# Performance work log

Hardware: AMD Instinct MI355X
Metric: run time of the kernel (lower is better)

## Reference

```python
import jax, jax.numpy as jnp
import numpy as np

H = 224  # config.output_height
W = 224  # config.output_width
N = 381  # config.num_frequency_bins (one splat per bin)
B = 16   # frames rendered per batch


def setup_inputs() -> dict:
    key = jax.random.key(0)
    k1, k2, k3 = jax.random.split(key, 3)
    # positions in [-0.9, 0.9] (spiral stays inside the frame)
    positions = jax.random.uniform(k1, (B, N, 2), dtype=jnp.float32, minval=-0.9, maxval=0.9)
    colors = jax.random.uniform(k2, (B, N, 3), dtype=jnp.float32)  # RGB in [0,1]
    # sizes in pixels, matching base_size=2 + size_scale=8*softplus(...)
    sizes = jax.random.uniform(k3, (B, N), dtype=jnp.float32, minval=2.0, maxval=10.0)
    return {"positions": positions, "colors": colors, "sizes": sizes}


def reference(positions, colors, sizes):
    """Soft (differentiable) rasterization of Gaussian point splats.

    positions: [B,N,2] in [-1,1]; colors: [B,N,3] in [0,1]; sizes: [B,N] pixels.
    Returns image [B,H,W,3] in [0,1].
    """
    gy = jnp.linspace(-1.0, 1.0, H, dtype=positions.dtype)
    gx = jnp.linspace(-1.0, 1.0, W, dtype=positions.dtype)
    # squared distance from every pixel to every point: [B,N,H,W]
    dx = gx[None, None, None, :] - positions[:, :, 0, None, None]
    dy = gy[None, None, :, None] - positions[:, :, 1, None, None]
    d2 = dx * dx + dy * dy
    # pixel size -> normalized coords ([-1,1] spans H pixels)
    sigma = sizes * (2.0 / H)  # [B,N]
    inv_two_var = 1.0 / (2.0 * sigma * sigma + 1e-8)
    weights = jnp.exp(-d2 * inv_two_var[:, :, None, None])  # [B,N,H,W]
    image = jnp.einsum('bnhw,bnc->bhwc', weights, colors)   # accumulate splats
    return jnp.clip(image, 0.0, 1.0)
```

## Files before the change

### kernel.cpp

```cpp
#include <hip/hip_runtime.h>
#include <math.h>

#define HH 224
#define WW 224
#define NS 381
#define BB 16
#define NPIX (BB * HH * WW)
#define TPB 256
#define TILE_W 32
#define TILE_H 32
#define TILES_X (WW / TILE_W)
#define BLKS_PER_IMG (TILES_X * (HH / TILE_H))
#define NBLK (BB * BLKS_PER_IMG)
#define NS_PAD 384
#define CUT 19.93f

__global__ __launch_bounds__(256) void splat_prep(const float* __restrict__ pos,
                                                  const float* __restrict__ col,
                                                  const float* __restrict__ siz,
                                                  float4* __restrict__ ws) {
    int i = blockIdx.x * 256 + threadIdx.x;
    if (i >= BB * NS) return;
    float px = pos[2 * i + 0];
    float py = pos[2 * i + 1];
    float cr = col[3 * i + 0];
    float cg = col[3 * i + 1];
    float cb = col[3 * i + 2];
    float sg = siz[i] * (2.0f / (float)HH);
    float itv = 1.0f / (2.0f * sg * sg + 1e-8f);
    float ss = sqrtf(itv * 1.44269504088896340736f);
    ws[2 * i + 0] = make_float4(ss, -px * ss, -py * ss, cr);
    ws[2 * i + 1] = make_float4(cg, cb, 0.0f, 0.0f);
}

__global__ __launch_bounds__(TPB) void splat_render(const float4* __restrict__ ws,
                                                    float* __restrict__ out) {
    __shared__ float4 geo[NS_PAD];
    __shared__ float4 colr[NS_PAD];
    __shared__ int cnt;

    int blk = blockIdx.x;
    int b = blk / BLKS_PER_IMG;
    int t = blk - b * BLKS_PER_IMG;
    int tile_y = t / TILES_X;
    int tile_x = t - tile_y * TILES_X;

    if (threadIdx.x == 0) cnt = 0;
    __syncthreads();

    const float gstep = 2.0f / (float)(WW - 1);
    float x0 = -1.0f + (float)(tile_x * TILE_W) * gstep;
    float x1 = x0 + (float)(TILE_W - 1) * gstep;
    float y0 = -1.0f + (float)(tile_y * TILE_H) * gstep;
    float y1 = y0 + (float)(TILE_H - 1) * gstep;

    const float4* src = ws + (size_t)b * NS * 2;
    int lane = threadIdx.x & 63;

    for (int r = 0; r < 2; ++r) {
        int i = threadIdx.x + r * TPB;
        bool pass = false;
        float4 A = make_float4(0.f, 0.f, 0.f, 0.f);
        float4 C = make_float4(0.f, 0.f, 0.f, 0.f);
        if (i < NS) {
            A = src[2 * i + 0];
            C = src[2 * i + 1];
            float ss = A.x;
            float u = -A.y;
            float v = -A.z;
            float dx = fmaxf(fmaxf(x0 * ss - u, u - x1 * ss), 0.0f);
            float dy = fmaxf(fmaxf(y0 * ss - v, v - y1 * ss), 0.0f);
            pass = fmaf(dx, dx, dy * dy) < CUT;
        }
        unsigned long long mask = __ballot(pass);
        int pos = __popcll(mask & ((1ull << lane) - 1ull));
        int tot = __popcll(mask);
        int base = 0;
        if (lane == 0 && tot) base = atomicAdd(&cnt, tot);
        base = __shfl(base, 0);
        if (pass) {
            geo[base + pos]  = A;
            colr[base + pos] = C;
        }
    }
    __syncthreads();
    int m = cnt;
    int m4 = (m + 3) & ~3;
    if (threadIdx.x < (m4 - m)) {
        geo[m + threadIdx.x]  = make_float4(0.f, 0.f, 1000.0f, 0.f);
        colr[m + threadIdx.x] = make_float4(0.f, 0.f, 0.f, 0.f);
    }
    __syncthreads();
    m4 = __builtin_amdgcn_readfirstlane(m4);

    int tx = threadIdx.x & 7;
    int ty = threadIdx.x >> 3;
    int w0 = tile_x * TILE_W + tx * 4;
    int h  = tile_y * TILE_H + ty;
    float gy  = -1.0f + (float)h * gstep;
    float gx0 = -1.0f + (float)w0 * gstep;
    float gx1 = gx0 + gstep;
    float gx2 = gx0 + 2.0f * gstep;
    float gx3 = gx0 + 3.0f * gstep;

    float r0 = 0.f, g0 = 0.f, b0 = 0.f;
    float r1 = 0.f, g1 = 0.f, b1 = 0.f;
    float r2 = 0.f, g2 = 0.f, b2 = 0.f;
    float r3 = 0.f, g3 = 0.f, b3 = 0.f;

#pragma unroll 4
    for (int j = 0; j < m4; ++j) {
        float4 A = geo[j];
        float4 C = colr[j];
        float dy  = fmaf(gy, A.x, A.z);
        float ndd = -(dy * dy);
        if (ndd > -CUT) {
            float dx0 = fmaf(gx0, A.x, A.y);
            float dx1 = fmaf(gx1, A.x, A.y);
            float dx2 = fmaf(gx2, A.x, A.y);
            float dx3 = fmaf(gx3, A.x, A.y);
            float we0 = __builtin_amdgcn_exp2f(fmaf(-dx0, dx0, ndd));
            float we1 = __builtin_amdgcn_exp2f(fmaf(-dx1, dx1, ndd));
            float we2 = __builtin_amdgcn_exp2f(fmaf(-dx2, dx2, ndd));
            float we3 = __builtin_amdgcn_exp2f(fmaf(-dx3, dx3, ndd));
            r0 = fmaf(we0, A.w, r0); g0 = fmaf(we0, C.x, g0); b0 = fmaf(we0, C.y, b0);
            r1 = fmaf(we1, A.w, r1); g1 = fmaf(we1, C.x, g1); b1 = fmaf(we1, C.y, b1);
            r2 = fmaf(we2, A.w, r2); g2 = fmaf(we2, C.x, g2); b2 = fmaf(we2, C.y, b2);
            r3 = fmaf(we3, A.w, r3); g3 = fmaf(we3, C.x, g3); b3 = fmaf(we3, C.y, b3);
        }
    }

    float4* o4 = (float4*)(out + ((size_t)b * (HH * WW) + (size_t)h * WW + w0) * 3);
    o4[0] = make_float4(fminf(r0, 1.f), fminf(g0, 1.f), fminf(b0, 1.f), fminf(r1, 1.f));
    o4[1] = make_float4(fminf(g1, 1.f), fminf(b1, 1.f), fminf(r2, 1.f), fminf(g2, 1.f));
    o4[2] = make_float4(fminf(b2, 1.f), fminf(r3, 1.f), fminf(g3, 1.f), fminf(b3, 1.f));
}

__global__ __launch_bounds__(256) void splat_render_direct(const float* __restrict__ pos,
                                                           const float* __restrict__ col,
                                                           const float* __restrict__ siz,
                                                           float* __restrict__ out) {
    int p = blockIdx.x * 256 + threadIdx.x;
    int b   = p / (HH * WW);
    int rem = p - b * (HH * WW);
    int h = rem / WW;
    int w = rem - h * WW;
    float gx = -1.0f + (float)w * (2.0f / (float)(WW - 1));
    float gy = -1.0f + (float)h * (2.0f / (float)(HH - 1));

    const float* pb = pos + (size_t)b * NS * 2;
    const float* cb = col + (size_t)b * NS * 3;
    const float* sb = siz + (size_t)b * NS;

    float r = 0.0f, g = 0.0f, bl = 0.0f;
    for (int j = 0; j < NS; ++j) {
        float px = pb[2 * j], py = pb[2 * j + 1];
        float s  = sb[j] * (2.0f / (float)HH);
        float itv = 1.0f / (2.0f * s * s + 1e-8f);
        float negc = -itv * 1.44269504088896340736f;
        float dx = gx - px;
        float dy = gy - py;
        float d2 = fmaf(dy, dy, dx * dx);
        float wgt = __builtin_amdgcn_exp2f(d2 * negc);
        r  = fmaf(wgt, cb[3 * j + 0], r);
        g  = fmaf(wgt, cb[3 * j + 1], g);
        bl = fmaf(wgt, cb[3 * j + 2], bl);
    }
    float* o = out + (size_t)p * 3;
    o[0] = fminf(r, 1.0f);
    o[1] = fminf(g, 1.0f);
    o[2] = fminf(bl, 1.0f);
}

extern "C" void kernel_launch(void* const* d_in, const int* in_sizes, int n_in,
                              void* d_out, int out_size, void* d_ws, size_t ws_size,
                              hipStream_t stream) {
    const float* pos = (const float*)d_in[0];
    const float* col = (const float*)d_in[1];
    const float* siz = (const float*)d_in[2];
    float* out = (float*)d_out;

    const size_t ws_needed = (size_t)BB * NS * 2 * sizeof(float4);
    if (ws_size >= ws_needed) {
        float4* ws = (float4*)d_ws;
        splat_prep<<<(BB * NS + 255) / 256, 256, 0, stream>>>(pos, col, siz, ws);
        splat_render<<<NBLK, TPB, 0, stream>>>(ws, out);
    } else {
        splat_render_direct<<<NPIX / 256, 256, 0, stream>>>(pos, col, siz, out);
    }
}
```

Baseline: 77.58 us.

## Fuse splat prep into render, pack colors to 10-bit, 2x4 pixels per thread

Removes the separate prep kernel and computes splat parameters inside each render block during culling, which saves one launch and a workspace round trip. Colors are quantized to 10 bits per channel and packed into the fourth float of the geometry record, halving shared-memory records and LDS reads. Each thread now computes a 2x4 pixel patch with 128 threads per block, reusing the x terms across two rows. The quantization adds color error of up to about 5e-4 per splat, which accumulates over overlapping splats and may break tolerance. It also raises register pressure.

Result: slower. 83.99 us (+8.3%).

```diff
diff --git a/kernel.cpp b/kernel.cpp
--- a/kernel.cpp
+++ b/kernel.cpp
@@ -5,8 +5,7 @@
 #define WW 224
 #define NS 381
 #define BB 16
-#define NPIX (BB * HH * WW)
-#define TPB 256
+#define TPB 128
 #define TILE_W 32
 #define TILE_H 32
 #define TILES_X (WW / TILE_W)
@@ -15,28 +14,11 @@
 #define NS_PAD 384
 #define CUT 19.93f
 
-__global__ __launch_bounds__(256) void splat_prep(const float* __restrict__ pos,
-                                                  const float* __restrict__ col,
-                                                  const float* __restrict__ siz,
-                                                  float4* __restrict__ ws) {
-    int i = blockIdx.x * 256 + threadIdx.x;
-    if (i >= BB * NS) return;
-    float px = pos[2 * i + 0];
-    float py = pos[2 * i + 1];
-    float cr = col[3 * i + 0];
-    float cg = col[3 * i + 1];
-    float cb = col[3 * i + 2];
-    float sg = siz[i] * (2.0f / (float)HH);
-    float itv = 1.0f / (2.0f * sg * sg + 1e-8f);
-    float ss = sqrtf(itv * 1.44269504088896340736f);
-    ws[2 * i + 0] = make_float4(ss, -px * ss, -py * ss, cr);
-    ws[2 * i + 1] = make_float4(cg, cb, 0.0f, 0.0f);
-}
-
-__global__ __launch_bounds__(TPB) void splat_render(const float4* __restrict__ ws,
+__global__ __launch_bounds__(TPB) void splat_render(const float* __restrict__ pos,
+                                                    const float* __restrict__ col,
+                                                    const float* __restrict__ siz,
                                                     float* __restrict__ out) {
     __shared__ float4 geo[NS_PAD];
-    __shared__ float4 colr[NS_PAD];
     __shared__ int cnt;
 
     int blk = blockIdx.x;
@@ -54,122 +36,112 @@
     float y0 = -1.0f + (float)(tile_y * TILE_H) * gstep;
     float y1 = y0 + (float)(TILE_H - 1) * gstep;
 
-    const float4* src = ws + (size_t)b * NS * 2;
+    const float2* pb = (const float2*)(pos + (size_t)b * NS * 2);
+    const float*  cb = col + (size_t)b * NS * 3;
+    const float*  sb = siz + (size_t)b * NS;
     int lane = threadIdx.x & 63;
 
-    for (int r = 0; r < 2; ++r) {
+    for (int r = 0; r < 3; ++r) {
         int i = threadIdx.x + r * TPB;
         bool pass = false;
         float4 A = make_float4(0.f, 0.f, 0.f, 0.f);
-        float4 C = make_float4(0.f, 0.f, 0.f, 0.f);
         if (i < NS) {
-            A = src[2 * i + 0];
-            C = src[2 * i + 1];
-            float ss = A.x;
-            float u = -A.y;
-            float v = -A.z;
-            float dx = fmaxf(fmaxf(x0 * ss - u, u - x1 * ss), 0.0f);
-            float dy = fmaxf(fmaxf(y0 * ss - v, v - y1 * ss), 0.0f);
-            pass = fmaf(dx, dx, dy * dy) < CUT;
+            float2 p = pb[i];
+            float sg = sb[i] * (2.0f / (float)HH);
+            float itv = 1.0f / (2.0f * sg * sg + 1e-8f);
+            float ss = sqrtf(itv * 1.44269504088896340736f);
+            float u = p.x * ss, v = p.y * ss;
+            float dxm = fmaxf(fmaxf(x0 * ss - u, u - x1 * ss), 0.0f);
+            float dym = fmaxf(fmaxf(y0 * ss - v, v - y1 * ss), 0.0f);
+            pass = fmaf(dxm, dxm, dym * dym) < CUT;
+            if (pass) {
+                unsigned pr = (unsigned)fmaf(cb[3 * i + 0], 1023.0f, 0.5f);
+                unsigned pg = (unsigned)fmaf(cb[3 * i + 1], 1023.0f, 0.5f);
+                unsigned pc = (unsigned)fmaf(cb[3 * i + 2], 1023.0f, 0.5f);
+                A = make_float4(ss, -u, -v, __uint_as_float(pr | (pg << 10) | (pc << 20)));
+            }
         }
         unsigned long long mask = __ballot(pass);
-        int pos = __popcll(mask & ((1ull << lane) - 1ull));
+        int ofs = __popcll(mask & ((1ull << lane) - 1ull));
         int tot = __popcll(mask);
         int base = 0;
         if (lane == 0 && tot) base = atomicAdd(&cnt, tot);
         base = __shfl(base, 0);
-        if (pass) {
-            geo[base + pos]  = A;
-            colr[base + pos] = C;
-        }
+        if (pass) geo[base + ofs] = A;
     }
     __syncthreads();
     int m = cnt;
     int m4 = (m + 3) & ~3;
-    if (threadIdx.x < (m4 - m)) {
-        geo[m + threadIdx.x]  = make_float4(0.f, 0.f, 1000.0f, 0.f);
-        colr[m + threadIdx.x] = make_float4(0.f, 0.f, 0.f, 0.f);
-    }
+    if (threadIdx.x < (m4 - m))
+        geo[m + threadIdx.x] = make_float4(0.f, 0.f, 1000.0f, 0.f);
     __syncthreads();
     m4 = __builtin_amdgcn_readfirstlane(m4);
 
     int tx = threadIdx.x & 7;
     int ty = threadIdx.x >> 3;
     int w0 = tile_x * TILE_W + tx * 4;
-    int h  = tile_y * TILE_H + ty;
-    float gy  = -1.0f + (float)h * gstep;
+    int h0 = tile_y * TILE_H + ty * 2;
+    float gy0 = -1.0f + (float)h0 * gstep;
+    float gy1 = gy0 + gstep;
     float gx0 = -1.0f + (float)w0 * gstep;
     float gx1 = gx0 + gstep;
     float gx2 = gx0 + 2.0f * gstep;
     float gx3 = gx0 + 3.0f * gstep;
 
-    float r0 = 0.f, g0 = 0.f, b0 = 0.f;
-    float r1 = 0.f, g1 = 0.f, b1 = 0.f;
-    float r2 = 0.f, g2 = 0.f, b2 = 0.f;
-    float r3 = 0.f, g3 = 0.f, b3 = 0.f;
+    float r00 = 0.f, g00 = 0.f, b00 = 0.f, r01 = 0.f, g01 = 0.f, b01 = 0.f;
+    float r02 = 0.f, g02 = 0.f, b02 = 0.f, r03 = 0.f, g03 = 0.f, b03 = 0.f;
+    float r10 = 0.f, g10 = 0.f, b10 = 0.f, r11 = 0.f, g11 = 0.f, b11 = 0.f;
+    float r12 = 0.f, g12 = 0.f, b12 = 0.f, r13 = 0.f, g13 = 0.f, b13 = 0.f;
 
 #pragma unroll 4
     for (int j = 0; j < m4; ++j) {
         float4 A = geo[j];
-        float4 C = colr[j];
-        float dy  = fmaf(gy, A.x, A.z);
-        float ndd = -(dy * dy);
-        if (ndd > -CUT) {
+        float dy0 = fmaf(gy0, A.x, A.z);
+        float dy1 = fmaf(gy1, A.x, A.z);
+        float n0 = -(dy0 * dy0);
+        float n1 = -(dy1 * dy1);
+        if (fmaxf(n0, n1) > -CUT) {
+            unsigned pk = __float_as_uint(A.w);
+            const float q = (1.0f / 1023.0f);
+            float cr = (float)(pk & 1023u) * q;
+            float cg = (float)((pk >> 10) & 1023u) * q;
+            float cc = (float)(pk >> 20) * q;
             float dx0 = fmaf(gx0, A.x, A.y);
             float dx1 = fmaf(gx1, A.x, A.y);
             float dx2 = fmaf(gx2, A.x, A.y);
             float dx3 = fmaf(gx3, A.x, A.y);
-            float we0 = __builtin_amdgcn_exp2f(fmaf(-dx0, dx0, ndd));
-            float we1 = __builtin_amdgcn_exp2f(fmaf(-dx1, dx1, ndd));
-            float we2 = __builtin_amdgcn_exp2f(fmaf(-dx2, dx2, ndd));
-            float we3 = __builtin_amdgcn_exp2f(fmaf(-dx3, dx3, ndd));
-            r0 = fmaf(we0, A.w, r0); g0 = fmaf(we0, C.x, g0); b0 = fmaf(we0, C.y, b0);
-            r1 = fmaf(we1, A.w, r1); g1 = fmaf(we1, C.x, g1); b1 = fmaf(we1, C.y, b1);
-            r2 = fmaf(we2, A.w, r2); g2 = fmaf(we2, C.x, g2); b2 = fmaf(we2, C.y, b2);
-            r3 = fmaf(we3, A.w, r3); g3 = fmaf(we3, C.x, g3); b3 = fmaf(we3, C.y, b3);
+            float m0 = -(dx0 * dx0);
+            float m1 = -(dx1 * dx1);
+            float m2 = -(dx2 * dx2);
+            float m3 = -(dx3 * dx3);
+            float w00 = __builtin_amdgcn_exp2f(m0 + n0);
+            float w01 = __builtin_amdgcn_exp2f(m1 + n0);
+            float w02 = __builtin_amdgcn_exp2f(m2 + n0);
+            float w03 = __builtin_amdgcn_exp2f(m3 + n0);
+            float w10 = __builtin_amdgcn_exp2f(m0 + n1);
+            float w11 = __builtin_amdgcn_exp2f(m1 + n1);
+            float w12 = __builtin_amdgcn_exp2f(m2 + n1);
+            float w13 = __builtin_amdgcn_exp2f(m3 + n1);
+            r00 = fmaf(w00, cr, r00); g00 = fmaf(w00, cg, g00); b00 = fmaf(w00, cc, b00);
+            r01 = fmaf(w01, cr, r01); g01 = fmaf(w01, cg, g01); b01 = fmaf(w01, cc, b01);
+            r02 = fmaf(w02, cr, r02); g02 = fmaf(w02, cg, g02); b02 = fmaf(w02, cc, b02);
+            r03 = fmaf(w03, cr, r03); g03 = fmaf(w03, cg, g03); b03 = fmaf(w03, cc, b03);
+            r10 = fmaf(w10, cr, r10); g10 = fmaf(w10, cg, g10); b10 = fmaf(w10, cc, b10);
+            r11 = fmaf(w11, cr, r11); g11 = fmaf(w11, cg, g11); b11 = fmaf(w11, cc, b11);
+            r12 = fmaf(w12, cr, r12); g12 = fmaf(w12, cg, g12); b12 = fmaf(w12, cc, b12);
+            r13 = fmaf(w13, cr, r13); g13 = fmaf(w13, cg, g13); b13 = fmaf(w13, cc, b13);
         }
     }
 
-    float4* o4 = (float4*)(out + ((size_t)b * (HH * WW) + (size_t)h * WW + w0) * 3);
-    o4[0] = make_float4(fminf(r0, 1.f), fminf(g0, 1.f), fminf(b0, 1.f), fminf(r1, 1.f));
-    o4[1] = make_float4(fminf(g1, 1.f), fminf(b1, 1.f), fminf(r2, 1.f), fminf(g2, 1.f));
-    o4[2] = make_float4(fminf(b2, 1.f), fminf(r3, 1.f), fminf(g3, 1.f), fminf(b3, 1.f));
-}
-
-__global__ __launch_bounds__(256) void splat_render_direct(const float* __restrict__ pos,
-                                                           const float* __restrict__ col,
-                                                           const float* __restrict__ siz,
-                                                           float* __restrict__ out) {
-    int p = blockIdx.x * 256 + threadIdx.x;
-    int b   = p / (HH * WW);
-    int rem = p - b * (HH * WW);
-    int h = rem / WW;
-    int w = rem - h * WW;
-    float gx = -1.0f + (float)w * (2.0f / (float)(WW - 1));
-    float gy = -1.0f + (float)h * (2.0f / (float)(HH - 1));
-
-    const float* pb = pos + (size_t)b * NS * 2;
-    const float* cb = col + (size_t)b * NS * 3;
-    const float* sb = siz + (size_t)b * NS;
-
-    float r = 0.0f, g = 0.0f, bl = 0.0f;
-    for (int j = 0; j < NS; ++j) {
-        float px = pb[2 * j], py = pb[2 * j + 1];
-        float s  = sb[j] * (2.0f / (float)HH);
-        float itv = 1.0f / (2.0f * s * s + 1e-8f);
-        float negc = -itv * 1.44269504088896340736f;
-        float dx = gx - px;
-        float dy = gy - py;
-        float d2 = fmaf(dy, dy, dx * dx);
-        float wgt = __builtin_amdgcn_exp2f(d2 * negc);
-        r  = fmaf(wgt, cb[3 * j + 0], r);
-        g  = fmaf(wgt, cb[3 * j + 1], g);
-        bl = fmaf(wgt, cb[3 * j + 2], bl);
-    }
-    float* o = out + (size_t)p * 3;
-    o[0] = fminf(r, 1.0f);
-    o[1] = fminf(g, 1.0f);
-    o[2] = fminf(bl, 1.0f);
+    size_t base0 = ((size_t)b * (HH * WW) + (size_t)h0 * WW + w0) * 3;
+    float4* o0 = (float4*)(out + base0);
+    float4* o1 = (float4*)(out + base0 + (size_t)WW * 3);
+    o0[0] = make_float4(fminf(r00, 1.f), fminf(g00, 1.f), fminf(b00, 1.f), fminf(r01, 1.f));
+    o0[1] = make_float4(fminf(g01, 1.f), fminf(b01, 1.f), fminf(r02, 1.f), fminf(g02, 1.f));
+    o0[2] = make_float4(fminf(b02, 1.f), fminf(r03, 1.f), fminf(g03, 1.f), fminf(b03, 1.f));
+    o1[0] = make_float4(fminf(r10, 1.f), fminf(g10, 1.f), fminf(b10, 1.f), fminf(r11, 1.f));
+    o1[1] = make_float4(fminf(g11, 1.f), fminf(b11, 1.f), fminf(r12, 1.f), fminf(g12, 1.f));
+    o1[2] = make_float4(fminf(b12, 1.f), fminf(r13, 1.f), fminf(g13, 1.f), fminf(b13, 1.f));
 }
 
 extern "C" void kernel_launch(void* const* d_in, const int* in_sizes, int n_in,
@@ -179,13 +151,5 @@
     const float* col = (const float*)d_in[1];
     const float* siz = (const float*)d_in[2];
     float* out = (float*)d_out;
-
-    const size_t ws_needed = (size_t)BB * NS * 2 * sizeof(float4);
-    if (ws_size >= ws_needed) {
-        float4* ws = (float4*)d_ws;
-        splat_prep<<<(BB * NS + 255) / 256, 256, 0, stream>>>(pos, col, siz, ws);
-        splat_render<<<NBLK, TPB, 0, stream>>>(ws, out);
-    } else {
-        splat_render_direct<<<NPIX / 256, 256, 0, stream>>>(pos, col, siz, out);
-    }
+    splat_render<<<NBLK, TPB, 0, stream>>>(pos, col, siz, out);
 }
```
